# Kernel optimization log

Hardware: AMD Instinct MI355X
Metric: run time of the kernel (lower is better)

The kernel has to match this reference:

```python
import jax, jax.numpy as jnp
import numpy as np

B = 1048576  # batch
N = 5        # number of parallel LSTMs
H = 2        # input_size == hidden_size
CLS = 24     # 5*H + 14 others
OUT = 5


def setup_inputs() -> dict:
    key = jax.random.key(0)
    ks = jax.random.split(key, 10)
    s = 0.1
    return {
        "seqs": jax.random.normal(ks[0], (N, 1, B, H), dtype=jnp.float32),
        "others": jax.random.normal(ks[1], (1, B, 14), dtype=jnp.float32),
        # stacked LSTM params (PyTorch layout: gates ordered i,f,g,o; 4H rows)
        "w_ih": jax.random.normal(ks[2], (N, 4 * H, H), dtype=jnp.float32) * s,
        "w_hh": jax.random.normal(ks[3], (N, 4 * H, H), dtype=jnp.float32) * s,  # unused for T=1, h0=0
        "b_ih": jax.random.normal(ks[4], (N, 4 * H), dtype=jnp.float32) * s,
        "b_hh": jax.random.normal(ks[5], (N, 4 * H), dtype=jnp.float32) * s,
        # classifier: Linear(24,24) -> ReLU -> Linear(24,5) -> Sigmoid (torch layout: y = x @ W.T + b)
        "w1": jax.random.normal(ks[6], (CLS, CLS), dtype=jnp.float32) * s,
        "b1": jax.random.normal(ks[7], (CLS,), dtype=jnp.float32) * s,
        "w2": jax.random.normal(ks[8], (OUT, CLS), dtype=jnp.float32) * s,
        "b2": jax.random.normal(ks[9], (OUT,), dtype=jnp.float32) * s,
    }


def reference(seqs, others, w_ih, w_hh, b_ih, b_hh, w1, b1, w2, b2):
    # Each LSTM sees a length-1 sequence with h0=c0=0, so the recurrent
    # matmul (w_hh @ h0) vanishes and a single fused step suffices.
    x = seqs[:, 0]                                    # [N, B, H]
    gates = jnp.einsum("nbh,ngh->nbg", x, w_ih) + (b_ih + b_hh)[:, None, :]  # [N, B, 4H]
    i, f, g, o = jnp.split(gates, 4, axis=-1)         # each [N, B, H]
    c = jax.nn.sigmoid(i) * jnp.tanh(g)               # f*c0 = 0
    h = jax.nn.sigmoid(o) * jnp.tanh(c)               # [N, B, H]
    # concat the 5 LSTM outputs (dim order 0..4) then 'others', along features
    feats = jnp.concatenate([h.transpose(1, 0, 2).reshape(B, N * H), others[0]], axis=-1)  # [B, 24]
    hidden = jax.nn.relu(feats @ w1.T + b1)           # [B, 24]
    return jax.nn.sigmoid(hidden @ w2.T + b2)         # [B, 5]
```

## Files before the change

kernel.cpp:

```cpp
#include <hip/hip_runtime.h>


constexpr int Bc = 1048576;
constexpr int Nc = 5;

typedef __attribute__((ext_vector_type(8))) short bf16x8;
typedef __attribute__((ext_vector_type(4))) float f32x4;

__device__ __forceinline__ unsigned cvtpk(float lo, float hi) {
    unsigned r;
    asm("v_cvt_pk_bf16_f32 %0, %1, %2" : "=v"(r) : "v"(lo), "v"(hi));
    return r;
}
__device__ __forceinline__ float fast_sigmoid(float x) {
    return __builtin_amdgcn_rcpf(1.0f + __expf(-x));
}
__device__ __forceinline__ float sigtanh(float a, float b) {
    float ea = __expf(-a);
    float eb = __expf(2.0f * b);
    return (eb - 1.0f) * __builtin_amdgcn_rcpf((eb + 1.0f) * (1.0f + ea));
}
__device__ __forceinline__ bf16x8 as_bf16(uint4 v) {
    union { uint4 u; bf16x8 b; } c; c.u = v; return c.b;
}
__device__ __forceinline__ bf16x8 pack_row8(const float* row, bool valid) {
    uint4 h = make_uint4(0u, 0u, 0u, 0u);
    if (valid) {
        float4 a = *reinterpret_cast<const float4*>(row);
        float4 b = *reinterpret_cast<const float4*>(row + 4);
        h.x = cvtpk(a.x, a.y);
        h.y = cvtpk(a.z, a.w);
        h.z = cvtpk(b.x, b.y);
        h.w = cvtpk(b.z, b.w);
    }
    return as_bf16(h);
}

__global__ __launch_bounds__(256) void fused_rnn_mlp_v6(
    const float* __restrict__ seqs,
    const float* __restrict__ others,
    const float* __restrict__ w_ih,
    const float* __restrict__ b_ih,
    const float* __restrict__ b_hh,
    const float* __restrict__ w1,
    const float* __restrict__ b1,
    const float* __restrict__ w2,
    const float* __restrict__ b2,
    float* __restrict__ out)
{
    __shared__ unsigned char lds_all[4 * 5120];
    const int tid  = threadIdx.x;
    const int lane = tid & 63;
    const int wid  = tid >> 6;
    const int qt   = lane >> 4;
    const int rlo  = lane & 15;
    unsigned char* wb = lds_all + wid * 5120;

    const int elem = blockIdx.x * 256 + tid;

    float2 x[Nc];
#pragma unroll
    for (int n = 0; n < Nc; n++)
        x[n] = *reinterpret_cast<const float2*>(seqs + ((size_t)n * Bc + elem) * 2);
    float2 oth[7];
    {
        const float2* op = reinterpret_cast<const float2*>(others + (size_t)elem * 14);
#pragma unroll
        for (int j = 0; j < 7; j++) oth[j] = op[j];
    }

    float f[24];
#pragma unroll
    for (int n = 0; n < Nc; n++) {
        const float* w = w_ih + n * 16;
        const float bi0 = b_ih[n*8+0] + b_hh[n*8+0];
        const float bi1 = b_ih[n*8+1] + b_hh[n*8+1];
        const float bg0 = b_ih[n*8+4] + b_hh[n*8+4];
        const float bg1 = b_ih[n*8+5] + b_hh[n*8+5];
        const float bo0 = b_ih[n*8+6] + b_hh[n*8+6];
        const float bo1 = b_ih[n*8+7] + b_hh[n*8+7];
        float gi0 = fmaf(x[n].x, w[0],  fmaf(x[n].y, w[1],  bi0));
        float gi1 = fmaf(x[n].x, w[2],  fmaf(x[n].y, w[3],  bi1));
        float gg0 = fmaf(x[n].x, w[8],  fmaf(x[n].y, w[9],  bg0));
        float gg1 = fmaf(x[n].x, w[10], fmaf(x[n].y, w[11], bg1));
        float go0 = fmaf(x[n].x, w[12], fmaf(x[n].y, w[13], bo0));
        float go1 = fmaf(x[n].x, w[14], fmaf(x[n].y, w[15], bo1));
        float c0 = sigtanh(gi0, gg0);
        float c1 = sigtanh(gi1, gg1);
        f[n*2+0] = sigtanh(go0, c0);
        f[n*2+1] = sigtanh(go1, c1);
    }
#pragma unroll
    for (int j = 0; j < 7; j++) {
        f[10 + 2*j]     = oth[j].x;
        f[10 + 2*j + 1] = oth[j].y;
    }

    {
        unsigned d[12];
#pragma unroll
        for (int p = 0; p < 12; p++) d[p] = cvtpk(f[2*p], f[2*p+1]);
        unsigned char* rp = wb + lane * 80;
        *reinterpret_cast<uint4*>(rp     ) = make_uint4(d[0], d[1], d[2],  d[3]);
        *reinterpret_cast<uint4*>(rp + 16) = make_uint4(d[4], d[5], d[6],  d[7]);
        *reinterpret_cast<uint4*>(rp + 32) = make_uint4(d[8], d[9], d[10], d[11]);
        *reinterpret_cast<uint4*>(rp + 48) = make_uint4(0u, 0u, 0u, 0u);
    }

    const int k0 = 8 * qt;
    bf16x8 A1[2], A2;
    float4 b1v[2], b2v;
#pragma unroll
    for (int mt = 0; mt < 2; mt++) {
        const int j = rlo + 16 * mt;
        A1[mt] = pack_row8(w1 + j * 24 + k0, (j < 24) && (k0 < 24));
        if (16*mt + 4*qt < 24) {
            b1v[mt] = *reinterpret_cast<const float4*>(b1 + 16*mt + 4*qt);
        } else {
            b1v[mt] = make_float4(0.0f, 0.0f, 0.0f, 0.0f);
        }
    }
    A2 = pack_row8(w2 + rlo * 24 + k0, (rlo < 5) && (k0 < 24));
    {
        b2v = (qt == 0) ? *reinterpret_cast<const float4*>(b2)
                        : make_float4(b2[4], 0.0f, 0.0f, 0.0f);
    }

#pragma unroll
    for (int nt = 0; nt < 4; nt++) {
        const bf16x8 Bv = as_bf16(*reinterpret_cast<const uint4*>(
            wb + (16*nt + rlo) * 80 + qt * 16));
#pragma unroll
        for (int mt = 0; mt < 2; mt++) {
            f32x4 a = { b1v[mt].x, b1v[mt].y, b1v[mt].z, b1v[mt].w };
            a = __builtin_amdgcn_mfma_f32_16x16x32_bf16(A1[mt], Bv, a, 0, 0, 0);
            const unsigned p0 = cvtpk(fmaxf(a[0], 0.0f), fmaxf(a[1], 0.0f));
            const unsigned p1 = cvtpk(fmaxf(a[2], 0.0f), fmaxf(a[3], 0.0f));
            *reinterpret_cast<uint2*>(wb + (16*nt + rlo) * 80 + (32*mt + 8*qt)) =
                make_uint2(p0, p1);
        }
    }

#pragma unroll
    for (int nt = 0; nt < 4; nt++) {
        const bf16x8 Bv = as_bf16(*reinterpret_cast<const uint4*>(
            wb + (16*nt + rlo) * 80 + qt * 16));
        f32x4 a = { b2v.x, b2v.y, b2v.z, b2v.w };
        a = __builtin_amdgcn_mfma_f32_16x16x32_bf16(A2, Bv, a, 0, 0, 0);
        if (qt == 0) {
            *reinterpret_cast<float4*>(wb + (16*nt + rlo) * 32) =
                make_float4(a[0], a[1], a[2], a[3]);
        } else if (qt == 1) {
            *reinterpret_cast<float*>(wb + (16*nt + rlo) * 32 + 16) = a[0];
        }
    }
    {
        const float4 v  = *reinterpret_cast<const float4*>(wb + lane * 32);
        const float  v4 = *reinterpret_cast<const float*>(wb + lane * 32 + 16);
        float* o = out + (size_t)elem * 5;
        o[0] = fast_sigmoid(v.x);
        o[1] = fast_sigmoid(v.y);
        o[2] = fast_sigmoid(v.z);
        o[3] = fast_sigmoid(v.w);
        o[4] = fast_sigmoid(v4);
    }
}

extern "C" void kernel_launch(void* const* d_in, const int* in_sizes, int n_in,
                              void* d_out, int out_size, void* d_ws, size_t ws_size,
                              hipStream_t stream) {
    const float* seqs   = (const float*)d_in[0];
    const float* others = (const float*)d_in[1];
    const float* w_ih   = (const float*)d_in[2];
    const float* b_ih   = (const float*)d_in[4];
    const float* b_hh   = (const float*)d_in[5];
    const float* w1     = (const float*)d_in[6];
    const float* b1     = (const float*)d_in[7];
    const float* w2     = (const float*)d_in[8];
    const float* b2     = (const float*)d_in[9];
    float* out = (float*)d_out;

    dim3 grid(Bc / 256), block(256);
    fused_rnn_mlp_v6<<<grid, block, 0, stream>>>(
        seqs, others, w_ih, b_ih, b_hh, w1, b1, w2, b2, out);
}
```

Measured before the change: 29.40 us.

## Replace LDS transposes with register shuffles and 32x32x16 MFMA

Removes the per-wave LDS staging buffers. The MLP now runs on 32x32x16 bf16 MFMAs, with activations kept as B-operand fragments built from cross-half lane shuffles instead of LDS writes and reads. Each wave processes two 32-element halves, and results are stored directly from the accumulators. This drops LDS traffic and shared memory use, which could also help occupancy. In exchange it adds shuffle and select work, uses more accumulator registers, and the output stores become less coalesced.

```diff
diff --git a/kernel.cpp b/kernel.cpp
--- a/kernel.cpp
+++ b/kernel.cpp
@@ -5,7 +5,7 @@
 constexpr int Nc = 5;
 
 typedef __attribute__((ext_vector_type(8))) short bf16x8;
-typedef __attribute__((ext_vector_type(4))) float f32x4;
+typedef __attribute__((ext_vector_type(16))) float f32x16;
 
 __device__ __forceinline__ unsigned cvtpk(float lo, float hi) {
     unsigned r;
@@ -20,23 +20,24 @@
     float eb = __expf(2.0f * b);
     return (eb - 1.0f) * __builtin_amdgcn_rcpf((eb + 1.0f) * (1.0f + ea));
 }
-__device__ __forceinline__ bf16x8 as_bf16(uint4 v) {
-    union { uint4 u; bf16x8 b; } c; c.u = v; return c.b;
+__device__ __forceinline__ bf16x8 mk_frag(unsigned a, unsigned b,
+                                          unsigned c, unsigned d) {
+    union { uint4 u; bf16x8 v; } x;
+    x.u = make_uint4(a, b, c, d);
+    return x.v;
 }
 __device__ __forceinline__ bf16x8 pack_row8(const float* row, bool valid) {
-    uint4 h = make_uint4(0u, 0u, 0u, 0u);
+    unsigned h0 = 0, h1 = 0, h2 = 0, h3 = 0;
     if (valid) {
         float4 a = *reinterpret_cast<const float4*>(row);
         float4 b = *reinterpret_cast<const float4*>(row + 4);
-        h.x = cvtpk(a.x, a.y);
-        h.y = cvtpk(a.z, a.w);
-        h.z = cvtpk(b.x, b.y);
-        h.w = cvtpk(b.z, b.w);
+        h0 = cvtpk(a.x, a.y); h1 = cvtpk(a.z, a.w);
+        h2 = cvtpk(b.x, b.y); h3 = cvtpk(b.z, b.w);
     }
-    return as_bf16(h);
+    return mk_frag(h0, h1, h2, h3);
 }
 
-__global__ __launch_bounds__(256) void fused_rnn_mlp_v6(
+__global__ __launch_bounds__(256) void fused_rnn_mlp_v9(
     const float* __restrict__ seqs,
     const float* __restrict__ others,
     const float* __restrict__ w_ih,
@@ -48,15 +49,12 @@
     const float* __restrict__ b2,
     float* __restrict__ out)
 {
-    __shared__ unsigned char lds_all[4 * 5120];
     const int tid  = threadIdx.x;
     const int lane = tid & 63;
-    const int wid  = tid >> 6;
-    const int qt   = lane >> 4;
-    const int rlo  = lane & 15;
-    unsigned char* wb = lds_all + wid * 5120;
-
+    const int lo31 = lane & 31;
+    const int kh   = lane >> 5;
     const int elem = blockIdx.x * 256 + tid;
+    const int wbase = blockIdx.x * 256 + (tid >> 6) * 64;
 
     float2 x[Nc];
 #pragma unroll
@@ -69,7 +67,7 @@
         for (int j = 0; j < 7; j++) oth[j] = op[j];
     }
 
-    float f[24];
+    unsigned d[12];
 #pragma unroll
     for (int n = 0; n < Nc; n++) {
         const float* w = w_ih + n * 16;
@@ -87,82 +85,88 @@
         float go1 = fmaf(x[n].x, w[14], fmaf(x[n].y, w[15], bo1));
         float c0 = sigtanh(gi0, gg0);
         float c1 = sigtanh(gi1, gg1);
-        f[n*2+0] = sigtanh(go0, c0);
-        f[n*2+1] = sigtanh(go1, c1);
+        d[n] = cvtpk(sigtanh(go0, c0), sigtanh(go1, c1));
     }
 #pragma unroll
-    for (int j = 0; j < 7; j++) {
-        f[10 + 2*j]     = oth[j].x;
-        f[10 + 2*j + 1] = oth[j].y;
+    for (int j = 0; j < 7; j++)
+        d[5 + j] = cvtpk(oth[j].x, oth[j].y);
+
+    unsigned sd[12];
+#pragma unroll
+    for (int i = 0; i < 12; i++) sd[i] = __shfl_xor(d[i], 32);
+
+    unsigned b0a[4], b1a[4], b0b[4], b1b[4];
+#pragma unroll
+    for (int i = 0; i < 4; i++) {
+        b0a[i] = kh ? sd[4+i] : d[i];
+        b1a[i] = kh ? d[4+i]  : sd[i];
+        b0b[i] = kh ? 0u      : d[8+i];
+        b1b[i] = kh ? 0u      : sd[8+i];
     }
 
-    {
-        unsigned d[12];
+    bf16x8 A1a = pack_row8(w1 + lo31 * 24 + 8 * kh, lo31 < 24);
+    bf16x8 A1b = pack_row8(w1 + lo31 * 24 + 16, (lo31 < 24) && (kh == 0));
+    bf16x8 A2a = pack_row8(w2 + lo31 * 24 + 8 * kh, lo31 < 5);
+    bf16x8 A2b = pack_row8(w2 + lo31 * 24 + 16, (lo31 < 5) && (kh == 0));
+
+    f32x16 c1z;
 #pragma unroll
-        for (int p = 0; p < 12; p++) d[p] = cvtpk(f[2*p], f[2*p+1]);
-        unsigned char* rp = wb + lane * 80;
-        *reinterpret_cast<uint4*>(rp     ) = make_uint4(d[0], d[1], d[2],  d[3]);
-        *reinterpret_cast<uint4*>(rp + 16) = make_uint4(d[4], d[5], d[6],  d[7]);
-        *reinterpret_cast<uint4*>(rp + 32) = make_uint4(d[8], d[9], d[10], d[11]);
-        *reinterpret_cast<uint4*>(rp + 48) = make_uint4(0u, 0u, 0u, 0u);
+    for (int r = 0; r < 16; r++) {
+        const int jb = (r & 3) + 8 * (r >> 2);
+        float v = 0.0f;
+        if (jb < 24) v = kh ? b1[jb + 4] : b1[jb];
+        if (jb >= 24) v = 0.0f;
+        c1z[r] = v;
     }
+    f32x16 accA = c1z, accB = c1z;
 
-    const int k0 = 8 * qt;
-    bf16x8 A1[2], A2;
-    float4 b1v[2], b2v;
-#pragma unroll
-    for (int mt = 0; mt < 2; mt++) {
-        const int j = rlo + 16 * mt;
-        A1[mt] = pack_row8(w1 + j * 24 + k0, (j < 24) && (k0 < 24));
-        if (16*mt + 4*qt < 24) {
-            b1v[mt] = *reinterpret_cast<const float4*>(b1 + 16*mt + 4*qt);
-        } else {
-            b1v[mt] = make_float4(0.0f, 0.0f, 0.0f, 0.0f);
-        }
-    }
-    A2 = pack_row8(w2 + rlo * 24 + k0, (rlo < 5) && (k0 < 24));
-    {
-        b2v = (qt == 0) ? *reinterpret_cast<const float4*>(b2)
-                        : make_float4(b2[4], 0.0f, 0.0f, 0.0f);
-    }
+    accA = __builtin_amdgcn_mfma_f32_32x32x16_bf16(
+        A1a, mk_frag(b0a[0], b0a[1], b0a[2], b0a[3]), accA, 0, 0, 0);
+    accA = __builtin_amdgcn_mfma_f32_32x32x16_bf16(
+        A1b, mk_frag(b0b[0], b0b[1], b0b[2], b0b[3]), accA, 0, 0, 0);
+    accB = __builtin_amdgcn_mfma_f32_32x32x16_bf16(
+        A1a, mk_frag(b1a[0], b1a[1], b1a[2], b1a[3]), accB, 0, 0, 0);
+    accB = __builtin_amdgcn_mfma_f32_32x32x16_bf16(
+        A1b, mk_frag(b1b[0], b1b[1], b1b[2], b1b[3]), accB, 0, 0, 0);
 
 #pragma unroll
-    for (int nt = 0; nt < 4; nt++) {
-        const bf16x8 Bv = as_bf16(*reinterpret_cast<const uint4*>(
-            wb + (16*nt + rlo) * 80 + qt * 16));
+    for (int t = 0; t < 2; t++) {
+        const f32x16 acc = t ? accB : accA;
+        unsigned p0 = cvtpk(fmaxf(acc[0],  0.f), fmaxf(acc[1],  0.f));
+        unsigned p1 = cvtpk(fmaxf(acc[2],  0.f), fmaxf(acc[3],  0.f));
+        unsigned p2 = cvtpk(fmaxf(acc[4],  0.f), fmaxf(acc[5],  0.f));
+        unsigned p3 = cvtpk(fmaxf(acc[6],  0.f), fmaxf(acc[7],  0.f));
+        unsigned p4 = cvtpk(fmaxf(acc[8],  0.f), fmaxf(acc[9],  0.f));
+        unsigned p5 = cvtpk(fmaxf(acc[10], 0.f), fmaxf(acc[11], 0.f));
+        const unsigned q0 = __shfl_xor(p0, 32);
+        const unsigned q1 = __shfl_xor(p1, 32);
+        const unsigned q2 = __shfl_xor(p2, 32);
+        const unsigned q3 = __shfl_xor(p3, 32);
+        const unsigned q4 = __shfl_xor(p4, 32);
+        const unsigned q5 = __shfl_xor(p5, 32);
+        const bf16x8 B2a = mk_frag(kh ? q2 : p0, kh ? q3 : p1,
+                                   kh ? p2 : q0, kh ? p3 : q1);
+        const bf16x8 B2b = mk_frag(kh ? 0u : p4, kh ? 0u : p5,
+                                   kh ? 0u : q4, kh ? 0u : q5);
+        f32x16 c2;
 #pragma unroll
-        for (int mt = 0; mt < 2; mt++) {
-            f32x4 a = { b1v[mt].x, b1v[mt].y, b1v[mt].z, b1v[mt].w };
-            a = __builtin_amdgcn_mfma_f32_16x16x32_bf16(A1[mt], Bv, a, 0, 0, 0);
-            const unsigned p0 = cvtpk(fmaxf(a[0], 0.0f), fmaxf(a[1], 0.0f));
-            const unsigned p1 = cvtpk(fmaxf(a[2], 0.0f), fmaxf(a[3], 0.0f));
-            *reinterpret_cast<uint2*>(wb + (16*nt + rlo) * 80 + (32*mt + 8*qt)) =
-                make_uint2(p0, p1);
+        for (int r = 0; r < 16; r++) c2[r] = 0.0f;
+        c2[0] = kh ? b2[4] : b2[0];
+        if (!kh) { c2[1] = b2[1]; c2[2] = b2[2]; c2[3] = b2[3]; }
+        c2 = __builtin_amdgcn_mfma_f32_32x32x16_bf16(A2a, B2a, c2, 0, 0, 0);
+        c2 = __builtin_amdgcn_mfma_f32_32x32x16_bf16(A2b, B2b, c2, 0, 0, 0);
+
+        const float s0 = fast_sigmoid(c2[0]);
+        const float s1 = fast_sigmoid(c2[1]);
+        const float s2 = fast_sigmoid(c2[2]);
+        const float s3 = fast_sigmoid(c2[3]);
+        const int et = wbase + t * 32 + lo31;
+        float* o = out + (size_t)et * 5;
+        if (kh == 0) {
+            o[0] = s0; o[1] = s1; o[2] = s2; o[3] = s3;
+        } else {
+            o[4] = s0;
         }
-    }
-
-#pragma unroll
-    for (int nt = 0; nt < 4; nt++) {
-        const bf16x8 Bv = as_bf16(*reinterpret_cast<const uint4*>(
-            wb + (16*nt + rlo) * 80 + qt * 16));
-        f32x4 a = { b2v.x, b2v.y, b2v.z, b2v.w };
-        a = __builtin_amdgcn_mfma_f32_16x16x32_bf16(A2, Bv, a, 0, 0, 0);
-        if (qt == 0) {
-            *reinterpret_cast<float4*>(wb + (16*nt + rlo) * 32) =
-                make_float4(a[0], a[1], a[2], a[3]);
-        } else if (qt == 1) {
-            *reinterpret_cast<float*>(wb + (16*nt + rlo) * 32 + 16) = a[0];
-        }
-    }
-    {
-        const float4 v  = *reinterpret_cast<const float4*>(wb + lane * 32);
-        const float  v4 = *reinterpret_cast<const float*>(wb + lane * 32 + 16);
-        float* o = out + (size_t)elem * 5;
-        o[0] = fast_sigmoid(v.x);
-        o[1] = fast_sigmoid(v.y);
-        o[2] = fast_sigmoid(v.z);
-        o[3] = fast_sigmoid(v.w);
-        o[4] = fast_sigmoid(v4);
     }
 }
 
@@ -181,6 +185,6 @@
     float* out = (float*)d_out;
 
     dim3 grid(Bc / 256), block(256);
-    fused_rnn_mlp_v6<<<grid, block, 0, stream>>>(
+    fused_rnn_mlp_v9<<<grid, block, 0, stream>>>(
         seqs, others, w_ih, b_ih, b_hh, w1, b1, w2, b2, out);
 }
```

After: 32.56 us. +10.7%, slower.
